# Kernel tuning notes

Measured on AMD Instinct MI355X. Metric: run time of the kernel, lower is better.

## Reference

```python
import jax, jax.numpy as jnp
import numpy as np

B, T, M, C, H = 2, 2048, 512, 512, 8
D = C // H
SCALE = 1.0 / np.sqrt(D).astype(np.float32)


def _linear_params(key, din, dout):
    kw, kb = jax.random.split(key)
    W = jax.random.normal(kw, (din, dout), jnp.float32) * 0.02
    b = jax.random.normal(kb, (dout,), jnp.float32) * 0.02
    return W, b


def setup_inputs() -> dict:
    key = jax.random.key(0)
    ks = jax.random.split(key, 8)
    x = jax.random.normal(ks[0], (B, T, C), jnp.float32)
    y = jax.random.normal(ks[1], (B, M, C), jnp.float32)
    # causal mask over the x (self / product-attn) axis, broadcasts to [B,H,T,T]
    attn_x_mask = jnp.tril(jnp.ones((T, T), jnp.int32))[None, None]
    Wqkv_x, bqkv_x = _linear_params(ks[2], C, 3 * C)
    Wqkv_y, bqkv_y = _linear_params(ks[3], C, 3 * C)
    Wgs, bgs = _linear_params(ks[4], C, C)
    Wgc, bgc = _linear_params(ks[5], C, C)
    Wp, bp = _linear_params(ks[6], C, C)
    return dict(x=x, y=y, attn_x_mask=attn_x_mask,
                Wqkv_x=Wqkv_x, bqkv_x=bqkv_x, Wqkv_y=Wqkv_y, bqkv_y=bqkv_y,
                Wgs=Wgs, bgs=bgs, Wgc=Wgc, bgc=bgc, Wp=Wp, bp=bp)


def _heads(t, L):
    # [B,L,C] -> [B,H,L,D]
    return t.reshape(B, L, H, D).transpose(0, 2, 1, 3)


def reference(x, y, attn_x_mask, Wqkv_x, bqkv_x, Wqkv_y, bqkv_y,
              Wgs, bgs, Wgc, bgc, Wp, bp):
    neg_inf = jnp.float32(-jnp.inf)
    qx, kx, vx = jnp.split(x @ Wqkv_x + bqkv_x, 3, axis=-1)
    qy, ky, vy = jnp.split(y @ Wqkv_y + bqkv_y, 3, axis=-1)
    q_x, k_x, v_x = _heads(qx, T), _heads(kx, T), _heads(vx, T)
    q_y, k_y, v_y = _heads(qy, M), _heads(ky, M), _heads(vy, M)

    # cross attention x -> y : [B,H,T,M]
    catt_x2y = jnp.einsum('bhtd,bhmd->bhtm', q_x, k_y) * SCALE
    cval_x2y = jnp.einsum('bhtm,bhmd->bhtd', jax.nn.softmax(catt_x2y, axis=-1), v_y)
    cval_x2y = cval_x2y.transpose(0, 2, 1, 3).reshape(B, T, C)

    # product attention: (x->y scores) @ (y->x scores) : [B,H,T,T]
    catt_y2x = jnp.einsum('bhmd,bhtd->bhmt', q_y, k_x) * SCALE
    prod = jnp.einsum('bhtm,bhms->bhts', catt_x2y, catt_y2x) * SCALE
    prod = jnp.where(attn_x_mask == 0, neg_inf, prod)
    cval_y2x = jnp.einsum('bhts,bhsd->bhtd', jax.nn.softmax(prod, axis=-1), v_x)
    cval_y2x = cval_y2x.transpose(0, 2, 1, 3).reshape(B, T, C)

    cval = cval_x2y + cval_y2x

    # self attention on x : [B,H,T,T]
    satt = jnp.einsum('bhtd,bhsd->bhts', q_x, k_x) * SCALE
    satt = jnp.where(attn_x_mask == 0, neg_inf, satt)
    sval = jnp.einsum('bhts,bhsd->bhtd', jax.nn.softmax(satt, axis=-1), v_x)
    sval = sval.transpose(0, 2, 1, 3).reshape(B, T, C)

    sgate = jax.nn.sigmoid(sval @ Wgs + bgs)
    cgate = jax.nn.sigmoid(cval @ Wgc + bgc)
    out = (sgate * cval + cgate * sval) @ Wp + bp
    return out
```

## Files before the change

kernel.cpp:

```cpp
#include <hip/hip_runtime.h>
#include <hip/hip_bf16.h>

typedef unsigned short ushort_t;
typedef __attribute__((ext_vector_type(8))) short s8v;
typedef __attribute__((ext_vector_type(4))) float f4;
typedef __attribute__((ext_vector_type(4))) unsigned short u16x4;

#define BB 2
#define TT 2048
#define MMM 512
#define CC 512
#define HH 8
#define DD 64
#define SCALE 0.125f
#define SCALE_L2E 0.18033688011112042f

__device__ __forceinline__ ushort_t f2bf(float v) {
    __hip_bfloat16 h = __float2bfloat16(v);
    return *reinterpret_cast<ushort_t*>(&h);
}
__device__ __forceinline__ float bf2f(ushort_t u) {
    __hip_bfloat16 h;
    *reinterpret_cast<ushort_t*>(&h) = u;
    return __bfloat162float(h);
// ... 135 lines not shown

    stage_rows128(Ab, 0, Al[0], w, lane);
    stage_rows128(Bb, 0, Bl[0], w, lane);
    __syncthreads();

    for (int kk = 0; kk < 8; ++kk) {
        const int cur = kk & 1;
        if (kk < 7) {
            stage_rows128(Ab, (kk + 1) * 64, Al[cur ^ 1], w, lane);
            stage_rows128(Bb, (kk + 1) * 64, Bl[cur ^ 1], w, lane);
        }
#pragma unroll
        for (int ks = 0; ks < 2; ++ks) {
            s8v af[4], bfr[4];
#pragma unroll
            for (int i = 0; i < 4; ++i) {
                int row = rowBase + 16 * i + l15;
                af[i] = *(const s8v*)&Al[cur][row * 64 + (((ks * 4 + quad) ^ (row & 7)) * 8)];
                int col = colBase + 16 * i + l15;
                bfr[i] = *(const s8v*)&Bl[cur][col * 64 + (((ks * 4 + quad) ^ (col & 7)) * 8)];
            }
#pragma unroll
            for (int i = 0; i < 4; ++i)
#pragma unroll
                for (int j = 0; j < 4; ++j)
                    acc[i][j] = __builtin_amdgcn_mfma_f32_16x16x32_bf16(af[i], bfr[j], acc[i][j], 0, 0, 0);
        }
        __syncthreads();
    }

#pragma unroll
    for (int i = 0; i < 4; ++i)
#pragma unroll
        for (int j = 0; j < 4; ++j)
#pragma unroll
            for (int r = 0; r < 4; ++r) {
                int row = r0 + rowBase + 16 * i + quad * 4 + r;
                int col = c0 + colBase + 16 * j + l15;
                float v = acc[i][j][r] + bias[col];
                if (col < qcols) v *= SCALE_L2E;
                O[(long)row * 1536 + col] = f2bf(v);
            }
}

__global__ __launch_bounds__(256) void proj_k(
    const ushort_t* __restrict__ A, const ushort_t* __restrict__ Bm,
    float* __restrict__ O, const float* __restrict__ bias)
{
    const int r0 = blockIdx.y * 64, c0 = blockIdx.x * 64;
    const int tid = threadIdx.x, w = tid >> 6, lane = tid & 63;
    const int quad = lane >> 4, l15 = lane & 15;
    const int rowBase = (w >> 1) * 32, colBase = (w & 1) * 32;

    __shared__ __align__(16) ushort_t Al[3][64 * 64];
    __shared__ __align__(16) ushort_t Bl[3][64 * 64];

    const ushort_t* Ab = A + (long)r0 * 512;
    const ushort_t* Bb = Bm + (long)c0 * 512;

    f4 acc[2][2] = {};

    stage_rows64(Ab, 0, Al[0], w, lane);
    stage_rows64(Bb, 0, Bl[0], w, lane);
    stage_rows64(Ab, 64, Al[1], w, lane);
    stage_rows64(Bb, 64, Bl[1], w, lane);

    int cur = 0;
    for (int kk = 0; kk < 8; ++kk) {
        if (kk + 1 < 8) asm volatile("s_waitcnt vmcnt(4)" ::: "memory");
        else            asm volatile("s_waitcnt vmcnt(0)" ::: "memory");
        asm volatile("s_barrier" ::: "memory");
        if (kk + 2 < 8) {
            int s = cur + 2; if (s >= 3) s -= 3;
            stage_rows64(Ab, (kk + 2) * 64, Al[s], w, lane);
            stage_rows64(Bb, (kk + 2) * 64, Bl[s], w, lane);
        }
#pragma unroll
        for (int ks = 0; ks < 2; ++ks) {
            s8v af[2], bfr[2];
#pragma unroll
            for (int i = 0; i < 2; ++i) {
                int row = rowBase + 16 * i + l15;
                af[i] = *(const s8v*)&Al[cur][row * 64 + (((ks * 4 + quad) ^ (row & 7)) * 8)];
                int col = colBase + 16 * i + l15;
                bfr[i] = *(const s8v*)&Bl[cur][col * 64 + (((ks * 4 + quad) ^ (col & 7)) * 8)];
            }
#pragma unroll
            for (int i = 0; i < 2; ++i)
#pragma unroll
                for (int j = 0; j < 2; ++j)
                    acc[i][j] = __builtin_amdgcn_mfma_f32_16x16x32_bf16(af[i], bfr[j], acc[i][j], 0, 0, 0);
        }
        if (++cur == 3) cur = 0;
    }

#pragma unroll
    for (int i = 0; i < 2; ++i)
#pragma unroll
        for (int j = 0; j < 2; ++j)
#pragma unroll
            for (int r = 0; r < 4; ++r) {
                int row = r0 + rowBase + 16 * i + quad * 4 + r;
                int col = c0 + colBase + 16 * j + l15;
                O[(long)row * 512 + col] = acc[i][j][r] + bias[col];
            }
}

__global__ __launch_bounds__(256) void gt_k(const ushort_t* __restrict__ qyT,
                                            const ushort_t* __restrict__ kyT,
                                            ushort_t* __restrict__ Gt)
{
    const int z = blockIdx.x;
    const int tid = threadIdx.x, w = tid >> 6, lane = tid & 63;
    const int quad = lane >> 4, l15 = lane & 15;
    const ushort_t* A  = qyT + (long)z * 64 * MMM;
    const ushort_t* Bm = kyT + (long)z * 64 * MMM;
    __shared__ float red[4][4096];
    f4 acc[4][4] = {};
    for (int kk = 0; kk < 4; ++kk) {
        const int ks = w * 4 + kk;
        s8v af[4], bfr[4];
#pragma unroll
        for (int i = 0; i < 4; ++i) {
            af[i]  = *(const s8v*)(A  + (long)(16 * i + l15) * MMM + ks * 32 + quad * 8);
            bfr[i] = *(const s8v*)(Bm + (long)(16 * i + l15) * MMM + ks * 32 + quad * 8);
        }
#pragma unroll
        for (int i = 0; i < 4; ++i)
#pragma unroll
            for (int j = 0; j < 4; ++j)
                acc[i][j] = __builtin_amdgcn_mfma_f32_16x16x32_bf16(af[i], bfr[j], acc[i][j], 0, 0, 0);
    }
#pragma unroll
    for (int i = 0; i < 4; ++i)
#pragma unroll
        for (int j = 0; j < 4; ++j)
            *(f4*)&red[w][(i * 4 + j) * 256 + lane * 4] = acc[i][j];
    __syncthreads();
    const float s2 = SCALE * SCALE;
#pragma unroll
    for (int j = 0; j < 4; ++j) {
        f4 s = *(const f4*)&red[0][(w * 4 + j) * 256 + lane * 4];
#pragma unroll
        for (int ww = 1; ww < 4; ++ww)
            s += *(const f4*)&red[ww][(w * 4 + j) * 256 + lane * 4];
#pragma unroll
        for (int r = 0; r < 4; ++r) {
            int d2 = 16 * w + quad * 4 + r, d1 = 16 * j + l15;
            Gt[(long)z * 4096 + d2 * 64 + d1] = f2bf(s2 * s[r]);
        }
    }
}

__device__ __forceinline__ void stage_k64(const ushort_t* src, long rstride, int s0,
                                          ushort_t* Kl, int w, int lane) {
#pragma unroll
    for (int n = 0; n < 2; ++n) {
        int f = w * 2048 + n * 1024 + lane * 16;
        int row = f >> 7;
        int krow = ((row & 15) << 2) | (row >> 4);
        int blk = ((f & 127) >> 4) ^ (row & 7);
        gload16(src + (long)(s0 + krow) * rstride + blk * 8, &Kl[(w * 2048 + n * 1024) >> 1]);
    }
}
__device__ __forceinline__ void stage_v64(const ushort_t* src, long rstride, int s0,
                                          ushort_t* Vl, int w, int lane) {
#pragma unroll
    for (int n = 0; n < 2; ++n) {
        int f = w * 2048 + n * 1024 + lane * 16;
        int row = f >> 7;
        int blk = ((f & 127) >> 4) ^ (row & 7);
        gload16(src + (long)row * rstride + s0 + blk * 8, &Vl[(w * 2048 + n * 1024) >> 1]);
    }
}
__device__ __forceinline__ void qk8(f4 Sc[4], const s8v qf[2], const ushort_t* Kl,
                                    int quad, int l15) {
    __builtin_amdgcn_s_setprio(1);
#pragma unroll
    for (int ks = 0; ks < 2; ++ks)
#pragma unroll
        for (int c = 0; c < 4; ++c) {
            int row = 16 * c + l15;
            s8v bb = *(const s8v*)&Kl[row * 64 + (((ks * 4 + quad) ^ (row & 7)) * 8)];
            Sc[c] = __builtin_amdgcn_mfma_f32_16x16x32_bf16(qf[ks], bb, Sc[c], 0, 0, 0);
        }
    __builtin_amdgcn_s_setprio(0);
}
__device__ __forceinline__ void qk8_dual(f4 Ss[4], f4 Sp[4], const s8v qa[2], const s8v qb[2],
                                         const ushort_t* Kl, int quad, int l15) {
    __builtin_amdgcn_s_setprio(1);
#pragma unroll
    for (int ks = 0; ks < 2; ++ks)
#pragma unroll
        for (int c = 0; c < 4; ++c) {
            int row = 16 * c + l15;
            s8v bb = *(const s8v*)&Kl[row * 64 + (((ks * 4 + quad) ^ (row & 7)) * 8)];
            Ss[c] = __builtin_amdgcn_mfma_f32_16x16x32_bf16(qa[ks], bb, Ss[c], 0, 0, 0);
            Sp[c] = __builtin_amdgcn_mfma_f32_16x16x32_bf16(qb[ks], bb, Sp[c], 0, 0, 0);
        }
    __builtin_amdgcn_s_setprio(0);
}
__device__ __forceinline__ void smax0(const f4 Sc[4], float l_i[4], ushort_t* PlW,
                                      int diag, int trow0, int s0, int quad, int l15) {
#pragma unroll
    for (int r = 0; r < 4; ++r) {
        const int trow = trow0 + quad * 4 + r;
        u16x4 o;
#pragma unroll
        for (int c = 0; c < 4; ++c) {
            float v = Sc[c][r];
            if (diag && (s0 + 4 * l15 + c) > trow) v = -3e38f;
            float p = exp2_raw(v);
            l_i[r] += p;
            o[c] = f2bf(p);
        }
        *(u16x4*)&PlW[(quad * 4 + r) * 72 + 4 * l15] = o;
    }
}
__device__ __forceinline__ void pv8(f4 Oc[4], const ushort_t* PlW, const ushort_t* Vl,
                                    int quad, int l15) {
    __builtin_amdgcn_s_setprio(1);
#pragma unroll
    for (int ks = 0; ks < 2; ++ks) {
        s8v a = *(const s8v*)&PlW[l15 * 72 + ks * 32 + quad * 8];
#pragma unroll
        for (int c = 0; c < 4; ++c) {
            int row = 16 * c + l15;
            s8v bb = *(const s8v*)&Vl[row * 64 + (((ks * 4 + quad) ^ (row & 7)) * 8)];
            Oc[c] = __builtin_amdgcn_mfma_f32_16x16x32_bf16(a, bb, Oc[c], 0, 0, 0);
        }
    }
    __builtin_amdgcn_s_setprio(0);
}
__device__ __forceinline__ void pv8_dual(f4 Os[4], f4 Op[4], const ushort_t* Ps,
                                         const ushort_t* Pp, const ushort_t* Vl,
                                         int quad, int l15) {
    __builtin_amdgcn_s_setprio(1);
#pragma unroll
    for (int ks = 0; ks < 2; ++ks) {
        s8v as = *(const s8v*)&Ps[l15 * 72 + ks * 32 + quad * 8];
        s8v ap = *(const s8v*)&Pp[l15 * 72 + ks * 32 + quad * 8];
#pragma unroll
        for (int c = 0; c < 4; ++c) {
            int row = 16 * c + l15;
            s8v bb = *(const s8v*)&Vl[row * 64 + (((ks * 4 + quad) ^ (row & 7)) * 8)];
            Os[c] = __builtin_amdgcn_mfma_f32_16x16x32_bf16(as, bb, Os[c], 0, 0, 0);
            Op[c] = __builtin_amdgcn_mfma_f32_16x16x32_bf16(ap, bb, Op[c], 0, 0, 0);
        }
    }
    __builtin_amdgcn_s_setprio(0);
}

__global__ __launch_bounds__(256, 2) void flash_fused(
    const ushort_t* __restrict__ qkvx, const ushort_t* __restrict__ qkvy,
    const ushort_t* __restrict__ Gt, const ushort_t* __restrict__ vxT,
    const ushort_t* __restrict__ vyT,
    ushort_t* __restrict__ cval, ushort_t* __restrict__ sval)
{
    const int z = blockIdx.y, b = z >> 3, h = z & 7;
    const ushort_t* qx = qkvx + (long)b * (TT * 1536) + h * 64;
    const ushort_t* kx = qx + 512;
    const ushort_t* ky = qkvy + (long)b * (MMM * 1536) + 512 + h * 64;
    const ushort_t* Gz = Gt + (long)z * 4096;
    const ushort_t* vx = vxT + (long)z * (64 * TT);
    const ushort_t* vy = vyT + (long)z * (64 * MMM);

    const int xw = (z & 8) ? (int)blockIdx.x : (int)(gridDim.x - 1 - blockIdx.x);
    const int t0 = xw * 64;
    const int tid = threadIdx.x, w = tid >> 6, lane = tid & 63;
    const int quad = lane >> 4, l15 = lane & 15;

    __shared__ __align__(16) ushort_t Kl[3][64 * 64];
    __shared__ __align__(16) ushort_t Vl[3][64 * 64];
    __shared__ __align__(16) ushort_t Pl[2][4 * 16 * 72];
    ushort_t* PlWs = &Pl[0][w * 1152];
    ushort_t* PlWp = &Pl[1][w * 1152];

    stage_k64(ky, 1536, 0, Kl[0], w, lane);
    stage_v64(vy, MMM, 0, Vl[0], w, lane);
    stage_k64(ky, 1536, 64, Kl[1], w, lane);
    stage_v64(vy, MMM, 64, Vl[1], w, lane);

    const int qrow = t0 + 16 * w + l15;
    s8v qfx[2], qft[2];
    qfx[0] = *(const s8v*)(qx + (long)qrow * 1536 + quad * 8);
    qfx[1] = *(const s8v*)(qx + (long)qrow * 1536 + 32 + quad * 8);
    {
        f4 qa[4] = {};
#pragma unroll
        for (int ks = 0; ks < 2; ++ks)
#pragma unroll
            for (int j = 0; j < 4; ++j) {
                s8v bb = *(const s8v*)(Gz + (4 * l15 + j) * 64 + ks * 32 + quad * 8);
                qa[j] = __builtin_amdgcn_mfma_f32_16x16x32_bf16(qfx[ks], bb, qa[j], 0, 0, 0);
            }
#pragma unroll
        for (int r = 0; r < 4; ++r) {
            u16x4 o;
#pragma unroll
            for (int j = 0; j < 4; ++j) o[j] = f2bf(qa[j][r]);
            *(u16x4*)&PlWs[(quad * 4 + r) * 72 + 4 * l15] = o;
        }
        qft[0] = *(const s8v*)&PlWs[l15 * 72 + quad * 8];
        qft[1] = *(const s8v*)&PlWs[l15 * 72 + 32 + quad * 8];
    }

    f4 Occ[4] = {}, Ocs[4] = {}, Ocp[4] = {};
    float lc[4] = {}, ls[4] = {}, lp[4] = {};

    const int nT1 = MMM / 64;
    const int nTiles = nT1 + t0 / 64 + 1;

    int cur = 0;
    for (int ti = 0; ti < nTiles; ++ti) {
        if (ti + 1 < nTiles) asm volatile("s_waitcnt vmcnt(4)" ::: "memory");
        else                 asm volatile("s_waitcnt vmcnt(0)" ::: "memory");
        asm volatile("s_barrier" ::: "memory");
        if (ti + 2 < nTiles) {
            int s = cur + 2; if (s >= 3) s -= 3;
            const int tn = ti + 2;
            if (tn < nT1) {
                stage_k64(ky, 1536, tn * 64, Kl[s], w, lane);
                stage_v64(vy, MMM, tn * 64, Vl[s], w, lane);
            } else {
                const int s0n = (tn - nT1) * 64;
                stage_k64(kx, 1536, s0n, Kl[s], w, lane);
                stage_v64(vx, TT, s0n, Vl[s], w, lane);
            }
        }
        if (ti < nT1) {
            f4 Sc[4] = {};
            qk8(Sc, qfx, Kl[cur], quad, l15);
            smax0(Sc, lc, PlWs, 0, 0, 0, quad, l15);
            pv8(Occ, PlWs, Vl[cur], quad, l15);
        } else {
            const int s0 = (ti - nT1) * 64;
            const int diag = (s0 == t0);
            f4 Ss[4] = {}, Sp[4] = {};
            qk8_dual(Ss, Sp, qfx, qft, Kl[cur], quad, l15);
            smax0(Ss, ls, PlWs, diag, t0 + 16 * w, s0, quad, l15);
            smax0(Sp, lp, PlWp, diag, t0 + 16 * w, s0, quad, l15);
            pv8_dual(Ocs, Ocp, PlWs, PlWp, Vl[cur], quad, l15);
        }
        if (++cur == 3) cur = 0;
    }

#pragma unroll
    for (int r = 0; r < 4; ++r)
#pragma unroll
        for (int mb = 1; mb < 16; mb <<= 1) {
            lc[r] += __shfl_xor(lc[r], mb, 64);
            ls[r] += __shfl_xor(ls[r], mb, 64);
            lp[r] += __shfl_xor(lp[r], mb, 64);
        }

    const long ob = (long)b * (TT * CC) + h * 64;
#pragma unroll
    for (int r = 0; r < 4; ++r) {
        int row = t0 + 16 * w + quad * 4 + r;
        float ic = 1.f / lc[r], ip = 1.f / lp[r], isv = 1.f / ls[r];
#pragma unroll
        for (int c = 0; c < 4; ++c) {
            long idx = ob + (long)row * CC + 16 * c + l15;
            cval[idx] = f2bf(Occ[c][r] * ic + Ocp[c][r] * ip);
            sval[idx] = f2bf(Ocs[c][r] * isv);
        }
    }
}

__global__ __launch_bounds__(256) void gate_gemm(
    const ushort_t* __restrict__ sval, const ushort_t* __restrict__ cvalb,
    const ushort_t* __restrict__ WgsT, const ushort_t* __restrict__ WgcT,
    const float* __restrict__ bgs, const float* __restrict__ bgc,
    ushort_t* __restrict__ tmpb)
{
    const int r0 = blockIdx.y * 64, c0 = blockIdx.x * 64;
    const int tid = threadIdx.x, w = tid >> 6, lane = tid & 63;
    const int quad = lane >> 4, l15 = lane & 15;
    const int rowBase = (w >> 1) * 32, colBase = (w & 1) * 32;

    __shared__ __align__(16) ushort_t Al[3][64 * 64];
    __shared__ __align__(16) ushort_t Bl[3][64 * 64];

    const ushort_t* Ap[2] = { sval + (long)r0 * 512, cvalb + (long)r0 * 512 };
    const ushort_t* Bp[2] = { WgsT + (long)c0 * 512, WgcT + (long)c0 * 512 };

    f4 acc1[2][2] = {}, acc2[2][2] = {};

    stage_rows64(Ap[0], 0, Al[0], w, lane);
    stage_rows64(Bp[0], 0, Bl[0], w, lane);
    stage_rows64(Ap[0], 64, Al[1], w, lane);
    stage_rows64(Bp[0], 64, Bl[1], w, lane);

    int cur = 0;
    for (int st = 0; st < 16; ++st) {
        if (st + 1 < 16) asm volatile("s_waitcnt vmcnt(4)" ::: "memory");
        else             asm volatile("s_waitcnt vmcnt(0)" ::: "memory");
        asm volatile("s_barrier" ::: "memory");
        if (st + 2 < 16) {
            int s = cur + 2; if (s >= 3) s -= 3;
            const int nx = st + 2, p = nx >> 3;
            stage_rows64(Ap[p], (nx & 7) * 64, Al[s], w, lane);
            stage_rows64(Bp[p], (nx & 7) * 64, Bl[s], w, lane);
        }
#pragma unroll
        for (int ks = 0; ks < 2; ++ks) {
            s8v af[2], bfr[2];
#pragma unroll
            for (int i = 0; i < 2; ++i) {
                int row = rowBase + 16 * i + l15;
                af[i] = *(const s8v*)&Al[cur][row * 64 + (((ks * 4 + quad) ^ (row & 7)) * 8)];
                int col = colBase + 16 * i + l15;
                bfr[i] = *(const s8v*)&Bl[cur][col * 64 + (((ks * 4 + quad) ^ (col & 7)) * 8)];
            }
            if (st < 8) {
#pragma unroll
                for (int i = 0; i < 2; ++i)
#pragma unroll
                    for (int j = 0; j < 2; ++j)
                        acc1[i][j] = __builtin_amdgcn_mfma_f32_16x16x32_bf16(af[i], bfr[j], acc1[i][j], 0, 0, 0);
            } else {
#pragma unroll
                for (int i = 0; i < 2; ++i)
#pragma unroll
                    for (int j = 0; j < 2; ++j)
                        acc2[i][j] = __builtin_amdgcn_mfma_f32_16x16x32_bf16(af[i], bfr[j], acc2[i][j], 0, 0, 0);
            }
        }
        if (++cur == 3) cur = 0;
    }

#pragma unroll
    for (int i = 0; i < 2; ++i)
#pragma unroll
        for (int j = 0; j < 2; ++j)
#pragma unroll
            for (int r = 0; r < 4; ++r) {
                int row = r0 + rowBase + 16 * i + quad * 4 + r;
                int col = c0 + colBase + 16 * j + l15;
                long idx = (long)row * 512 + col;
                float g1 = 1.f / (1.f + __expf(-(acc1[i][j][r] + bgs[col])));
                float g2 = 1.f / (1.f + __expf(-(acc2[i][j][r] + bgc[col])));
                tmpb[idx] = f2bf(g1 * bf2f(cvalb[idx]) + g2 * bf2f(sval[idx]));
            }
}

extern "C" void kernel_launch(void* const* d_in, const int* in_sizes, int n_in,
                              void* d_out, int out_size, void* d_ws, size_t ws_size,
                              hipStream_t stream) {
    const float* x      = (const float*)d_in[0];
    const float* y      = (const float*)d_in[1];
    const float* Wqkv_x = (const float*)d_in[3];
    const float* bqkv_x = (const float*)d_in[4];
    const float* Wqkv_y = (const float*)d_in[5];
    const float* bqkv_y = (const float*)d_in[6];
    const float* Wgs    = (const float*)d_in[7];
    const float* bgs    = (const float*)d_in[8];
    const float* Wgc    = (const float*)d_in[9];
    const float* bgc    = (const float*)d_in[10];
    const float* Wp     = (const float*)d_in[11];
    const float* bp     = (const float*)d_in[12];
    float* out = (float*)d_out;

    ushort_t* u = (ushort_t*)d_ws;
    long o = 0;
    ushort_t* xb    = u + o; o += (long)BB * TT * CC;
    ushort_t* yb    = u + o; o += (long)BB * MMM * CC;
    ushort_t* WqxT  = u + o; o += 1536L * 512;
    ushort_t* WqyT  = u + o; o += 1536L * 512;
    ushort_t* WgsT  = u + o; o += 512L * 512;
    ushort_t* WgcT  = u + o; o += 512L * 512;
    ushort_t* WpT   = u + o; o += 512L * 512;
    ushort_t* qkvx  = u + o; o += (long)BB * TT * 1536;
    ushort_t* qkvy  = u + o; o += (long)BB * MMM * 1536;
    ushort_t* vxT   = u + o; o += (long)BB * HH * DD * TT;
    ushort_t* vyT   = u + o; o += (long)BB * HH * DD * MMM;
    ushort_t* kyT   = u + o; o += (long)BB * HH * DD * MMM;
    ushort_t* qyT   = u + o; o += (long)BB * HH * DD * MMM;
    ushort_t* Gt    = u + o; o += 16L * 64 * 64;
    ushort_t* cvalb = u + o; o += (long)BB * TT * CC;
    ushort_t* sval  = u + o; o += (long)BB * TT * CC;
    ushort_t* tmpb  = u + o; o += (long)BB * TT * CC;

    dim3 blk(256);

    prep_k<<<dim3(4864), blk, 0, stream>>>(x, y, Wqkv_x, Wqkv_y, Wgs, Wgc, Wp,
                                           xb, yb, WqxT, WqyT, WgsT, WgcT, WpT);

    qkv_k<<<dim3(12, 40), blk, 0, stream>>>(xb, yb, WqxT, WqyT, bqkv_x, bqkv_y, qkvx, qkvy);

    vT_fused<<<dim3(56, 16), blk, 0, stream>>>(qkvx, qkvy, vxT, vyT, kyT, qyT);

    gt_k<<<dim3(16), blk, 0, stream>>>(qyT, kyT, Gt);

    flash_fused<<<dim3(32, 16), blk, 0, stream>>>(qkvx, qkvy, Gt, vxT, vyT, cvalb, sval);

    gate_gemm<<<dim3(8, 64), blk, 0, stream>>>(sval, cvalb, WgsT, WgcT, bgs, bgc, tmpb);

    proj_k<<<dim3(8, 64), blk, 0, stream>>>(tmpb, WpT, out, bp);
}
```

Baseline: 206.6 us.

## Balance causal flash work by pairing query tiles and splitting long tiles

Each block now handles a short query tile (qA) plus part of its mirrored long tile (qB = 31 - p), so every block processes the same number of KV tiles. The long tile's work is split across two blocks, which write unnormalized partial outputs and row sums to fp32 scratch. A new combine kernel sums the two partials, normalizes, and writes cval and sval. This targets tail imbalance from the causal triangle, at the cost of an extra launch, fp32 partial traffic, and a second Q-fragment and Gt setup per block.

```diff
diff --git a/kernel.cpp b/kernel.cpp
--- a/kernel.cpp
+++ b/kernel.cpp
@@ -409,14 +409,111 @@
     }
     __builtin_amdgcn_s_setprio(0);
 }
+__device__ __forceinline__ void reduce16(float (&a)[4], float (&b)[4], float (&c)[4]) {
+#pragma unroll
+    for (int r = 0; r < 4; ++r)
+#pragma unroll
+        for (int mb = 1; mb < 16; mb <<= 1) {
+            a[r] += __shfl_xor(a[r], mb, 64);
+            b[r] += __shfl_xor(b[r], mb, 64);
+            c[r] += __shfl_xor(c[r], mb, 64);
+        }
+}
+
+__device__ __forceinline__ void run_chunk(
+    const ushort_t* ky, const ushort_t* vy, const ushort_t* kx, const ushort_t* vx,
+    const ushort_t* qx, const ushort_t* Gz,
+    ushort_t (*Kl)[64 * 64], ushort_t (*Vl)[64 * 64],
+    ushort_t* PlWs, ushort_t* PlWp,
+    int qt, int c0, int nc, int u0, int nu,
+    int w, int lane, int quad, int l15,
+    f4 (&Occ)[4], f4 (&Ocs)[4], f4 (&Ocp)[4],
+    float (&lc)[4], float (&ls)[4], float (&lp)[4])
+{
+    const int n = nc + nu;
+    const int t0q = qt * 64;
+    auto stage = [&](int ti, int slot) {
+        if (ti < nc) {
+            const int c = c0 + ti;
+            stage_k64(ky, 1536, c * 64, Kl[slot], w, lane);
+            stage_v64(vy, MMM, c * 64, Vl[slot], w, lane);
+        } else {
+            const int uu = u0 + ti - nc;
+            stage_k64(kx, 1536, uu * 64, Kl[slot], w, lane);
+            stage_v64(vx, TT, uu * 64, Vl[slot], w, lane);
+        }
+    };
+    stage(0, 0);
+    stage(1, 1);
+
+    const int qrow = t0q + 16 * w + l15;
+    s8v qfx[2], qft[2];
+    qfx[0] = *(const s8v*)(qx + (long)qrow * 1536 + quad * 8);
+    qfx[1] = *(const s8v*)(qx + (long)qrow * 1536 + 32 + quad * 8);
+    if (nu > 0) {
+        f4 qa[4] = {};
+#pragma unroll
+        for (int ks = 0; ks < 2; ++ks)
+#pragma unroll
+            for (int j = 0; j < 4; ++j) {
+                s8v bb = *(const s8v*)(Gz + (4 * l15 + j) * 64 + ks * 32 + quad * 8);
+                qa[j] = __builtin_amdgcn_mfma_f32_16x16x32_bf16(qfx[ks], bb, qa[j], 0, 0, 0);
+            }
+#pragma unroll
+        for (int r = 0; r < 4; ++r) {
+            u16x4 o;
+#pragma unroll
+            for (int j = 0; j < 4; ++j) o[j] = f2bf(qa[j][r]);
+            *(u16x4*)&PlWs[(quad * 4 + r) * 72 + 4 * l15] = o;
+        }
+        qft[0] = *(const s8v*)&PlWs[l15 * 72 + quad * 8];
+        qft[1] = *(const s8v*)&PlWs[l15 * 72 + 32 + quad * 8];
+    } else {
+        qft[0] = qfx[0]; qft[1] = qfx[1];
+    }
+    asm volatile("s_waitcnt vmcnt(0)" ::: "memory");
+    asm volatile("s_barrier" ::: "memory");
+
+    int cur = 0;
+    for (int ti = 0; ti < n; ++ti) {
+        if (ti > 0) {
+            if (ti + 1 < n) asm volatile("s_waitcnt vmcnt(4)" ::: "memory");
+            else            asm volatile("s_waitcnt vmcnt(0)" ::: "memory");
+            asm volatile("s_barrier" ::: "memory");
+        }
+        if (ti + 2 < n) {
+            int sl = cur + 2; if (sl >= 3) sl -= 3;
+            stage(ti + 2, sl);
+        }
+        if (ti < nc) {
+            f4 Sc[4] = {};
+            qk8(Sc, qfx, Kl[cur], quad, l15);
+            smax0(Sc, lc, PlWs, 0, 0, 0, quad, l15);
+            pv8(Occ, PlWs, Vl[cur], quad, l15);
+        } else {
+            const int uu = u0 + ti - nc;
+            const int diag = (uu == qt);
+            f4 Ss[4] = {}, Sp[4] = {};
+            qk8_dual(Ss, Sp, qfx, qft, Kl[cur], quad, l15);
+            smax0(Ss, ls, PlWs, diag, t0q + 16 * w, uu * 64, quad, l15);
+            smax0(Sp, lp, PlWp, diag, t0q + 16 * w, uu * 64, quad, l15);
+            pv8_dual(Ocs, Ocp, PlWs, PlWp, Vl[cur], quad, l15);
+        }
+        if (++cur == 3) cur = 0;
+    }
+    asm volatile("s_barrier" ::: "memory");
+}
 
 __global__ __launch_bounds__(256, 2) void flash_fused(
     const ushort_t* __restrict__ qkvx, const ushort_t* __restrict__ qkvy,
     const ushort_t* __restrict__ Gt, const ushort_t* __restrict__ vxT,
     const ushort_t* __restrict__ vyT,
-    ushort_t* __restrict__ cval, ushort_t* __restrict__ sval)
+    ushort_t* __restrict__ cval, ushort_t* __restrict__ sval,
+    float* __restrict__ partO, float* __restrict__ partL)
 {
     const int z = blockIdx.y, b = z >> 3, h = z & 7;
+    const int sblk = blockIdx.x, p = sblk >> 1, half = sblk & 1;
+    const int qA = p, qB = 31 - p;
     const ushort_t* qx = qkvx + (long)b * (TT * 1536) + h * 64;
     const ushort_t* kx = qx + 512;
     const ushort_t* ky = qkvy + (long)b * (MMM * 1536) + 512 + h * 64;
@@ -424,8 +521,6 @@
     const ushort_t* vx = vxT + (long)z * (64 * TT);
     const ushort_t* vy = vyT + (long)z * (64 * MMM);
 
-    const int xw = (z & 8) ? (int)blockIdx.x : (int)(gridDim.x - 1 - blockIdx.x);
-    const int t0 = xw * 64;
     const int tid = threadIdx.x, w = tid >> 6, lane = tid & 63;
     const int quad = lane >> 4, l15 = lane & 15;
 
@@ -435,95 +530,111 @@
     ushort_t* PlWs = &Pl[0][w * 1152];
     ushort_t* PlWp = &Pl[1][w * 1152];
 
-    stage_k64(ky, 1536, 0, Kl[0], w, lane);
-    stage_v64(vy, MMM, 0, Vl[0], w, lane);
-    stage_k64(ky, 1536, 64, Kl[1], w, lane);
-    stage_v64(vy, MMM, 64, Vl[1], w, lane);
-
-    const int qrow = t0 + 16 * w + l15;
-    s8v qfx[2], qft[2];
-    qfx[0] = *(const s8v*)(qx + (long)qrow * 1536 + quad * 8);
-    qfx[1] = *(const s8v*)(qx + (long)qrow * 1536 + 32 + quad * 8);
-    {
-        f4 qa[4] = {};
-#pragma unroll
-        for (int ks = 0; ks < 2; ++ks)
-#pragma unroll
-            for (int j = 0; j < 4; ++j) {
-                s8v bb = *(const s8v*)(Gz + (4 * l15 + j) * 64 + ks * 32 + quad * 8);
-                qa[j] = __builtin_amdgcn_mfma_f32_16x16x32_bf16(qfx[ks], bb, qa[j], 0, 0, 0);
-            }
+    int cA2, uA2;
+    if (p >= 12) { cA2 = 32 - 2 * p; uA2 = 0; }
+    else         { cA2 = 8;          uA2 = 12 - p; }
+
+    const long obase = (long)b * (TT * CC) + h * 64;
+    const long inst = (long)z * 16 + (qB - 16);
+    float* po = partO + (inst * 2 + half) * 3 * 4096;
+    float* pl = partL + (inst * 2 + half) * 3 * 64;
+
+    if (half == 0) {
+        {
+            f4 Occ[4] = {}, Ocs[4] = {}, Ocp[4] = {};
+            float lc[4] = {}, ls[4] = {}, lp[4] = {};
+            run_chunk(ky, vy, kx, vx, qx, Gz, Kl, Vl, PlWs, PlWp,
+                      qA, 0, 8, 0, qA + 1, w, lane, quad, l15,
+                      Occ, Ocs, Ocp, lc, ls, lp);
+            reduce16(lc, ls, lp);
+#pragma unroll
+            for (int r = 0; r < 4; ++r) {
+                int row = qA * 64 + 16 * w + quad * 4 + r;
+                float ic = 1.f / lc[r], ip = 1.f / lp[r], isv = 1.f / ls[r];
+#pragma unroll
+                for (int c = 0; c < 4; ++c) {
+                    long idx = obase + (long)row * CC + 16 * c + l15;
+                    cval[idx] = f2bf(Occ[c][r] * ic + Ocp[c][r] * ip);
+                    sval[idx] = f2bf(Ocs[c][r] * isv);
+                }
+            }
+        }
+        {
+            f4 Occ[4] = {}, Ocs[4] = {}, Ocp[4] = {};
+            float lc[4] = {}, ls[4] = {}, lp[4] = {};
+            run_chunk(ky, vy, kx, vx, qx, Gz, Kl, Vl, PlWs, PlWp,
+                      qB, 0, cA2, 0, uA2, w, lane, quad, l15,
+                      Occ, Ocs, Ocp, lc, ls, lp);
+            reduce16(lc, ls, lp);
+#pragma unroll
+            for (int r = 0; r < 4; ++r) {
+                const int row = 16 * w + quad * 4 + r;
+#pragma unroll
+                for (int c = 0; c < 4; ++c) {
+                    const int col = 16 * c + l15;
+                    po[row * 64 + col]        = Occ[c][r];
+                    po[4096 + row * 64 + col] = Ocs[c][r];
+                    po[8192 + row * 64 + col] = Ocp[c][r];
+                }
+                if (l15 == 0) { pl[row] = lc[r]; pl[64 + row] = ls[r]; pl[128 + row] = lp[r]; }
+            }
+        }
+    } else {
+        f4 Occ[4] = {}, Ocs[4] = {}, Ocp[4] = {};
+        float lc[4] = {}, ls[4] = {}, lp[4] = {};
+        run_chunk(ky, vy, kx, vx, qx, Gz, Kl, Vl, PlWs, PlWp,
+                  qB, cA2, 8 - cA2, uA2, (qB + 1) - uA2, w, lane, quad, l15,
+                  Occ, Ocs, Ocp, lc, ls, lp);
+        reduce16(lc, ls, lp);
 #pragma unroll
         for (int r = 0; r < 4; ++r) {
-            u16x4 o;
-#pragma unroll
-            for (int j = 0; j < 4; ++j) o[j] = f2bf(qa[j][r]);
-            *(u16x4*)&PlWs[(quad * 4 + r) * 72 + 4 * l15] = o;
-        }
-        qft[0] = *(const s8v*)&PlWs[l15 * 72 + quad * 8];
-        qft[1] = *(const s8v*)&PlWs[l15 * 72 + 32 + quad * 8];
-    }
-
-    f4 Occ[4] = {}, Ocs[4] = {}, Ocp[4] = {};
-    float lc[4] = {}, ls[4] = {}, lp[4] = {};
-
-    const int nT1 = MMM / 64;
-    const int nTiles = nT1 + t0 / 64 + 1;
-
-    int cur = 0;
-    for (int ti = 0; ti < nTiles; ++ti) {
-        if (ti + 1 < nTiles) asm volatile("s_waitcnt vmcnt(4)" ::: "memory");
-        else                 asm volatile("s_waitcnt vmcnt(0)" ::: "memory");
-        asm volatile("s_barrier" ::: "memory");
-        if (ti + 2 < nTiles) {
-            int s = cur + 2; if (s >= 3) s -= 3;
-            const int tn = ti + 2;
-            if (tn < nT1) {
-                stage_k64(ky, 1536, tn * 64, Kl[s], w, lane);
-                stage_v64(vy, MMM, tn * 64, Vl[s], w, lane);
-            } else {
-                const int s0n = (tn - nT1) * 64;
-                stage_k64(kx, 1536, s0n, Kl[s], w, lane);
-                stage_v64(vx, TT, s0n, Vl[s], w, lane);
-            }
-        }
-        if (ti < nT1) {
-            f4 Sc[4] = {};
-            qk8(Sc, qfx, Kl[cur], quad, l15);
-            smax0(Sc, lc, PlWs, 0, 0, 0, quad, l15);
-            pv8(Occ, PlWs, Vl[cur], quad, l15);
-        } else {
-            const int s0 = (ti - nT1) * 64;
-            const int diag = (s0 == t0);
-            f4 Ss[4] = {}, Sp[4] = {};
-            qk8_dual(Ss, Sp, qfx, qft, Kl[cur], quad, l15);
-            smax0(Ss, ls, PlWs, diag, t0 + 16 * w, s0, quad, l15);
-            smax0(Sp, lp, PlWp, diag, t0 + 16 * w, s0, quad, l15);
-            pv8_dual(Ocs, Ocp, PlWs, PlWp, Vl[cur], quad, l15);
-        }
-        if (++cur == 3) cur = 0;
-    }
-
-#pragma unroll
-    for (int r = 0; r < 4; ++r)
-#pragma unroll
-        for (int mb = 1; mb < 16; mb <<= 1) {
-            lc[r] += __shfl_xor(lc[r], mb, 64);
-            ls[r] += __shfl_xor(ls[r], mb, 64);
-            lp[r] += __shfl_xor(lp[r], mb, 64);
-        }
-
-    const long ob = (long)b * (TT * CC) + h * 64;
-#pragma unroll
-    for (int r = 0; r < 4; ++r) {
-        int row = t0 + 16 * w + quad * 4 + r;
-        float ic = 1.f / lc[r], ip = 1.f / lp[r], isv = 1.f / ls[r];
-#pragma unroll
-        for (int c = 0; c < 4; ++c) {
-            long idx = ob + (long)row * CC + 16 * c + l15;
-            cval[idx] = f2bf(Occ[c][r] * ic + Ocp[c][r] * ip);
-            sval[idx] = f2bf(Ocs[c][r] * isv);
-        }
+            const int row = 16 * w + quad * 4 + r;
+#pragma unroll
+            for (int c = 0; c < 4; ++c) {
+                const int col = 16 * c + l15;
+                po[row * 64 + col]        = Occ[c][r];
+                po[4096 + row * 64 + col] = Ocs[c][r];
+                po[8192 + row * 64 + col] = Ocp[c][r];
+            }
+            if (l15 == 0) { pl[row] = lc[r]; pl[64 + row] = ls[r]; pl[128 + row] = lp[r]; }
+        }
+    }
+}
+
+__global__ __launch_bounds__(256) void combine_k(
+    const float* __restrict__ partO, const float* __restrict__ partL,
+    ushort_t* __restrict__ cval, ushort_t* __restrict__ sval)
+{
+    const int inst = blockIdx.x;
+    const int z = inst >> 4, qb = 16 + (inst & 15);
+    const int b = z >> 3, h = z & 7;
+    const int tid = threadIdx.x;
+    const int row = tid >> 2, cq = (tid & 3) * 16;
+    const float* p0 = partO + ((long)inst * 2 + 0) * 3 * 4096;
+    const float* p1 = partO + ((long)inst * 2 + 1) * 3 * 4096;
+    const float* l0 = partL + ((long)inst * 2 + 0) * 3 * 64;
+    const float* l1 = partL + ((long)inst * 2 + 1) * 3 * 64;
+    const float ic  = 1.f / (l0[row] + l1[row]);
+    const float isv = 1.f / (l0[64 + row] + l1[64 + row]);
+    const float ip  = 1.f / (l0[128 + row] + l1[128 + row]);
+    const long ob = (long)b * (TT * CC) + h * 64 + (long)(qb * 64 + row) * CC + cq;
+    u16x4 vc[4], vs[4];
+#pragma unroll
+    for (int k = 0; k < 4; ++k) {
+        const int e = row * 64 + cq + k * 4;
+        f4 oc = *(const f4*)&p0[e]        + *(const f4*)&p1[e];
+        f4 os = *(const f4*)&p0[4096 + e] + *(const f4*)&p1[4096 + e];
+        f4 op = *(const f4*)&p0[8192 + e] + *(const f4*)&p1[8192 + e];
+#pragma unroll
+        for (int j = 0; j < 4; ++j) {
+            vc[k][j] = f2bf(oc[j] * ic + op[j] * ip);
+            vs[k][j] = f2bf(os[j] * isv);
+        }
+    }
+#pragma unroll
+    for (int k = 0; k < 4; ++k) {
+        *(u16x4*)&cval[ob + k * 4] = vc[k];
+        *(u16x4*)&sval[ob + k * 4] = vs[k];
     }
 }
 
@@ -640,6 +751,8 @@
     ushort_t* cvalb = u + o; o += (long)BB * TT * CC;
     ushort_t* sval  = u + o; o += (long)BB * TT * CC;
     ushort_t* tmpb  = u + o; o += (long)BB * TT * CC;
+    float* partO = (float*)(u + o); o += 256L * 2 * 3 * 4096 * 2;
+    float* partL = (float*)(u + o); o += 256L * 2 * 3 * 64 * 2;
 
     dim3 blk(256);
 
@@ -652,7 +765,10 @@
 
     gt_k<<<dim3(16), blk, 0, stream>>>(qyT, kyT, Gt);
 
-    flash_fused<<<dim3(32, 16), blk, 0, stream>>>(qkvx, qkvy, Gt, vxT, vyT, cvalb, sval);
+    flash_fused<<<dim3(32, 16), blk, 0, stream>>>(qkvx, qkvy, Gt, vxT, vyT,
+                                                  cvalb, sval, partO, partL);
+
+    combine_k<<<dim3(256), blk, 0, stream>>>(partO, partL, cvalb, sval);
 
     gate_gemm<<<dim3(8, 64), blk, 0, stream>>>(sval, cvalb, WgsT, WgcT, bgs, bgc, tmpb);
 
```

Measured after the change: 218.3 us. 1.06x slower.

## Pair causal query tiles per 512-thread block to balance flash attention work

Applied to the files above, without the earlier changes.

The flash kernel now runs 512-thread blocks in which two 4-wave groups handle query tiles p and 31-p, so every block does the same amount of causal work. The groups share the K/V tiles staged in LDS. Past the shorter tile's diagonal, group 0 switches to the self-attention half of the longer tile while group 1 handles the product half, and the partial accumulators are combined through LDS at the end. This targets the load imbalance of the triangular causal loop and cuts redundant K/V loads for the shared y-tiles, at the cost of a more complex schedule and fewer blocks in flight.

```diff
diff --git a/kernel.cpp b/kernel.cpp
--- a/kernel.cpp
+++ b/kernel.cpp
@@ -311,26 +311,20 @@
     }
 }
 
-__device__ __forceinline__ void stage_k64(const ushort_t* src, long rstride, int s0,
-                                          ushort_t* Kl, int w, int lane) {
-#pragma unroll
-    for (int n = 0; n < 2; ++n) {
-        int f = w * 2048 + n * 1024 + lane * 16;
-        int row = f >> 7;
-        int krow = ((row & 15) << 2) | (row >> 4);
-        int blk = ((f & 127) >> 4) ^ (row & 7);
-        gload16(src + (long)(s0 + krow) * rstride + blk * 8, &Kl[(w * 2048 + n * 1024) >> 1]);
-    }
-}
-__device__ __forceinline__ void stage_v64(const ushort_t* src, long rstride, int s0,
-                                          ushort_t* Vl, int w, int lane) {
-#pragma unroll
-    for (int n = 0; n < 2; ++n) {
-        int f = w * 2048 + n * 1024 + lane * 16;
-        int row = f >> 7;
-        int blk = ((f & 127) >> 4) ^ (row & 7);
-        gload16(src + (long)row * rstride + s0 + blk * 8, &Vl[(w * 2048 + n * 1024) >> 1]);
-    }
+__device__ __forceinline__ void stage_k8(const ushort_t* src, long rstride, int s0,
+                                         ushort_t* Kl, int w2, int lane) {
+    int f = w2 * 1024 + lane * 16;
+    int row = f >> 7;
+    int krow = ((row & 15) << 2) | (row >> 4);
+    int blk = ((f & 127) >> 4) ^ (row & 7);
+    gload16(src + (long)(s0 + krow) * rstride + blk * 8, &Kl[(w2 * 1024) >> 1]);
+}
+__device__ __forceinline__ void stage_v8(const ushort_t* src, long rstride, int s0,
+                                         ushort_t* Vl, int w2, int lane) {
+    int f = w2 * 1024 + lane * 16;
+    int row = f >> 7;
+    int blk = ((f & 127) >> 4) ^ (row & 7);
+    gload16(src + (long)row * rstride + s0 + blk * 8, &Vl[(w2 * 1024) >> 1]);
 }
 __device__ __forceinline__ void qk8(f4 Sc[4], const s8v qf[2], const ushort_t* Kl,
                                     int quad, int l15) {
@@ -409,14 +403,25 @@
     }
     __builtin_amdgcn_s_setprio(0);
 }
-
-__global__ __launch_bounds__(256, 2) void flash_fused(
+__device__ __forceinline__ void reduce16(float (&a)[4], float (&b)[4], float (&c)[4]) {
+#pragma unroll
+    for (int r = 0; r < 4; ++r)
+#pragma unroll
+        for (int mb = 1; mb < 16; mb <<= 1) {
+            a[r] += __shfl_xor(a[r], mb, 64);
+            b[r] += __shfl_xor(b[r], mb, 64);
+            c[r] += __shfl_xor(c[r], mb, 64);
+        }
+}
+
+__global__ __launch_bounds__(512, 2) void flash_fused(
     const ushort_t* __restrict__ qkvx, const ushort_t* __restrict__ qkvy,
     const ushort_t* __restrict__ Gt, const ushort_t* __restrict__ vxT,
     const ushort_t* __restrict__ vyT,
     ushort_t* __restrict__ cval, ushort_t* __restrict__ sval)
 {
     const int z = blockIdx.y, b = z >> 3, h = z & 7;
+    const int p = blockIdx.x;
     const ushort_t* qx = qkvx + (long)b * (TT * 1536) + h * 64;
     const ushort_t* kx = qx + 512;
     const ushort_t* ky = qkvy + (long)b * (MMM * 1536) + 512 + h * 64;
@@ -424,27 +429,28 @@
     const ushort_t* vx = vxT + (long)z * (64 * TT);
     const ushort_t* vy = vyT + (long)z * (64 * MMM);
 
-    const int xw = (z & 8) ? (int)blockIdx.x : (int)(gridDim.x - 1 - blockIdx.x);
-    const int t0 = xw * 64;
-    const int tid = threadIdx.x, w = tid >> 6, lane = tid & 63;
+    const int tid = threadIdx.x, w2 = tid >> 6, lane = tid & 63;
+    const int g = w2 >> 2, w = w2 & 3;
     const int quad = lane >> 4, l15 = lane & 15;
+    const int qB = 31 - p;
+    const int qg = g ? qB : p;
 
     __shared__ __align__(16) ushort_t Kl[3][64 * 64];
     __shared__ __align__(16) ushort_t Vl[3][64 * 64];
-    __shared__ __align__(16) ushort_t Pl[2][4 * 16 * 72];
-    ushort_t* PlWs = &Pl[0][w * 1152];
-    ushort_t* PlWp = &Pl[1][w * 1152];
-
-    stage_k64(ky, 1536, 0, Kl[0], w, lane);
-    stage_v64(vy, MMM, 0, Vl[0], w, lane);
-    stage_k64(ky, 1536, 64, Kl[1], w, lane);
-    stage_v64(vy, MMM, 64, Vl[1], w, lane);
-
-    const int qrow = t0 + 16 * w + l15;
+    __shared__ __align__(16) ushort_t Pl[2][8 * 16 * 72];
+    ushort_t* PlWs = &Pl[0][w2 * 1152];
+    ushort_t* PlWp = &Pl[1][w2 * 1152];
+
+    stage_k8(ky, 1536, 0, Kl[0], w2, lane);
+    stage_v8(vy, MMM, 0, Vl[0], w2, lane);
+    stage_k8(ky, 1536, 64, Kl[1], w2, lane);
+    stage_v8(vy, MMM, 64, Vl[1], w2, lane);
+
     s8v qfx[2], qft[2];
-    qfx[0] = *(const s8v*)(qx + (long)qrow * 1536 + quad * 8);
-    qfx[1] = *(const s8v*)(qx + (long)qrow * 1536 + 32 + quad * 8);
     {
+        const int qrow = qg * 64 + 16 * w + l15;
+        qfx[0] = *(const s8v*)(qx + (long)qrow * 1536 + quad * 8);
+        qfx[1] = *(const s8v*)(qx + (long)qrow * 1536 + 32 + quad * 8);
         f4 qa[4] = {};
 #pragma unroll
         for (int ks = 0; ks < 2; ++ks)
@@ -463,66 +469,112 @@
         qft[0] = *(const s8v*)&PlWs[l15 * 72 + quad * 8];
         qft[1] = *(const s8v*)&PlWs[l15 * 72 + 32 + quad * 8];
     }
+    asm volatile("s_waitcnt vmcnt(0)" ::: "memory");
+    asm volatile("s_barrier" ::: "memory");
 
     f4 Occ[4] = {}, Ocs[4] = {}, Ocp[4] = {};
     float lc[4] = {}, ls[4] = {}, lp[4] = {};
 
-    const int nT1 = MMM / 64;
-    const int nTiles = nT1 + t0 / 64 + 1;
-
+    const long obase = (long)b * (TT * CC) + h * 64;
+    const int n = 40 - p;
     int cur = 0;
-    for (int ti = 0; ti < nTiles; ++ti) {
-        if (ti + 1 < nTiles) asm volatile("s_waitcnt vmcnt(4)" ::: "memory");
-        else                 asm volatile("s_waitcnt vmcnt(0)" ::: "memory");
-        asm volatile("s_barrier" ::: "memory");
-        if (ti + 2 < nTiles) {
+    for (int ti = 0; ti < n; ++ti) {
+        if (ti > 0) {
+            if (ti + 1 < n) asm volatile("s_waitcnt vmcnt(2)" ::: "memory");
+            else            asm volatile("s_waitcnt vmcnt(0)" ::: "memory");
+            asm volatile("s_barrier" ::: "memory");
+        }
+        if (ti + 2 < n) {
             int s = cur + 2; if (s >= 3) s -= 3;
             const int tn = ti + 2;
-            if (tn < nT1) {
-                stage_k64(ky, 1536, tn * 64, Kl[s], w, lane);
-                stage_v64(vy, MMM, tn * 64, Vl[s], w, lane);
+            if (tn < 8) {
+                stage_k8(ky, 1536, tn * 64, Kl[s], w2, lane);
+                stage_v8(vy, MMM, tn * 64, Vl[s], w2, lane);
             } else {
-                const int s0n = (tn - nT1) * 64;
-                stage_k64(kx, 1536, s0n, Kl[s], w, lane);
-                stage_v64(vx, TT, s0n, Vl[s], w, lane);
-            }
-        }
-        if (ti < nT1) {
+                const int u = tn - 8;
+                stage_k8(kx, 1536, u * 64, Kl[s], w2, lane);
+                stage_v8(vx, TT, u * 64, Vl[s], w2, lane);
+            }
+        }
+        if (ti < 8) {
             f4 Sc[4] = {};
             qk8(Sc, qfx, Kl[cur], quad, l15);
             smax0(Sc, lc, PlWs, 0, 0, 0, quad, l15);
             pv8(Occ, PlWs, Vl[cur], quad, l15);
         } else {
-            const int s0 = (ti - nT1) * 64;
-            const int diag = (s0 == t0);
-            f4 Ss[4] = {}, Sp[4] = {};
-            qk8_dual(Ss, Sp, qfx, qft, Kl[cur], quad, l15);
-            smax0(Ss, ls, PlWs, diag, t0 + 16 * w, s0, quad, l15);
-            smax0(Sp, lp, PlWp, diag, t0 + 16 * w, s0, quad, l15);
-            pv8_dual(Ocs, Ocp, PlWs, PlWp, Vl[cur], quad, l15);
+            const int u = ti - 8;
+            if (u <= p) {
+                const int diag = (u == qg);
+                f4 Ss[4] = {}, Sp[4] = {};
+                qk8_dual(Ss, Sp, qfx, qft, Kl[cur], quad, l15);
+                smax0(Ss, ls, PlWs, diag, qg * 64 + 16 * w, u * 64, quad, l15);
+                smax0(Sp, lp, PlWp, diag, qg * 64 + 16 * w, u * 64, quad, l15);
+                pv8_dual(Ocs, Ocp, PlWs, PlWp, Vl[cur], quad, l15);
+            } else {
+                const int diag = (u == qB);
+                if (g == 0) {
+                    f4 Ss[4] = {};
+                    qk8(Ss, qfx, Kl[cur], quad, l15);
+                    smax0(Ss, ls, PlWs, diag, qB * 64 + 16 * w, u * 64, quad, l15);
+                    pv8(Ocs, PlWs, Vl[cur], quad, l15);
+                } else {
+                    f4 Sp[4] = {};
+                    qk8(Sp, qft, Kl[cur], quad, l15);
+                    smax0(Sp, lp, PlWp, diag, qB * 64 + 16 * w, u * 64, quad, l15);
+                    pv8(Ocp, PlWp, Vl[cur], quad, l15);
+                }
+            }
+            if (u == p && g == 0) {
+                reduce16(lc, ls, lp);
+#pragma unroll
+                for (int r = 0; r < 4; ++r) {
+                    int row = p * 64 + 16 * w + quad * 4 + r;
+                    float ic = 1.f / lc[r], ip = 1.f / lp[r], isv = 1.f / ls[r];
+#pragma unroll
+                    for (int c = 0; c < 4; ++c) {
+                        long idx = obase + (long)row * CC + 16 * c + l15;
+                        cval[idx] = f2bf(Occ[c][r] * ic + Ocp[c][r] * ip);
+                        sval[idx] = f2bf(Ocs[c][r] * isv);
+                    }
+                }
+#pragma unroll
+                for (int c = 0; c < 4; ++c) Ocs[c] = f4{};
+#pragma unroll
+                for (int r = 0; r < 4; ++r) ls[r] = 0.f;
+                const int qrow2 = qB * 64 + 16 * w + l15;
+                qfx[0] = *(const s8v*)(qx + (long)qrow2 * 1536 + quad * 8);
+                qfx[1] = *(const s8v*)(qx + (long)qrow2 * 1536 + 32 + quad * 8);
+            }
         }
         if (++cur == 3) cur = 0;
     }
 
-#pragma unroll
-    for (int r = 0; r < 4; ++r)
-#pragma unroll
-        for (int mb = 1; mb < 16; mb <<= 1) {
-            lc[r] += __shfl_xor(lc[r], mb, 64);
-            ls[r] += __shfl_xor(ls[r], mb, 64);
-            lp[r] += __shfl_xor(lp[r], mb, 64);
-        }
-
-    const long ob = (long)b * (TT * CC) + h * 64;
-#pragma unroll
-    for (int r = 0; r < 4; ++r) {
-        int row = t0 + 16 * w + quad * 4 + r;
-        float ic = 1.f / lc[r], ip = 1.f / lp[r], isv = 1.f / ls[r];
-#pragma unroll
-        for (int c = 0; c < 4; ++c) {
-            long idx = ob + (long)row * CC + 16 * c + l15;
-            cval[idx] = f2bf(Occ[c][r] * ic + Ocp[c][r] * ip);
-            sval[idx] = f2bf(Ocs[c][r] * isv);
+    __syncthreads();
+    float* comb = (float*)&Kl[0][0];
+    const int cbase = (w * 64 + lane) * 20;
+    if (g == 0) {
+#pragma unroll
+        for (int c = 0; c < 4; ++c) *(f4*)&comb[cbase + 4 * c] = Ocs[c];
+#pragma unroll
+        for (int r = 0; r < 4; ++r) comb[cbase + 16 + r] = ls[r];
+    }
+    __syncthreads();
+    if (g == 1) {
+#pragma unroll
+        for (int c = 0; c < 4; ++c) Ocs[c] += *(const f4*)&comb[cbase + 4 * c];
+#pragma unroll
+        for (int r = 0; r < 4; ++r) ls[r] += comb[cbase + 16 + r];
+        reduce16(lc, ls, lp);
+#pragma unroll
+        for (int r = 0; r < 4; ++r) {
+            int row = qB * 64 + 16 * w + quad * 4 + r;
+            float ic = 1.f / lc[r], ip = 1.f / lp[r], isv = 1.f / ls[r];
+#pragma unroll
+            for (int c = 0; c < 4; ++c) {
+                long idx = obase + (long)row * CC + 16 * c + l15;
+                cval[idx] = f2bf(Occ[c][r] * ic + Ocp[c][r] * ip);
+                sval[idx] = f2bf(Ocs[c][r] * isv);
+            }
         }
     }
 }
@@ -652,7 +704,8 @@
 
     gt_k<<<dim3(16), blk, 0, stream>>>(qyT, kyT, Gt);
 
-    flash_fused<<<dim3(32, 16), blk, 0, stream>>>(qkvx, qkvy, Gt, vxT, vyT, cvalb, sval);
+    flash_fused<<<dim3(16, 16), dim3(512), 0, stream>>>(qkvx, qkvy, Gt, vxT, vyT,
+                                                        cvalb, sval);
 
     gate_gemm<<<dim3(8, 64), blk, 0, stream>>>(sval, cvalb, WgsT, WgcT, bgs, bgc, tmpb);
 
```

New measurement: 215.8 us. 4.4% more time.

## Switch K/V staging to double buffer and preload V fragments into registers

Applied to the files above, without the earlier changes.

Reduces the shared K/V ring from three stages to two and replaces the manual vmcnt wait plus raw barrier with __syncthreads, prefetching only one tile ahead. V fragments are read from LDS into registers right after QK so their latency overlaps the softmax. The smaller LDS footprint may allow more resident blocks, but the shorter prefetch distance and the full syncthreads wait on every iteration can expose global-load latency. Holding the V fragments also raises register pressure.

```diff
diff --git a/kernel.cpp b/kernel.cpp
--- a/kernel.cpp
+++ b/kernel.cpp
@@ -359,6 +359,15 @@
         }
     __builtin_amdgcn_s_setprio(0);
 }
+__device__ __forceinline__ void vload8(s8v vf[8], const ushort_t* Vl, int quad, int l15) {
+#pragma unroll
+    for (int ks = 0; ks < 2; ++ks)
+#pragma unroll
+        for (int c = 0; c < 4; ++c) {
+            int row = 16 * c + l15;
+            vf[ks * 4 + c] = *(const s8v*)&Vl[row * 64 + (((ks * 4 + quad) ^ (row & 7)) * 8)];
+        }
+}
 __device__ __forceinline__ void smax0(const f4 Sc[4], float l_i[4], ushort_t* PlW,
                                       int diag, int trow0, int s0, int quad, int l15) {
 #pragma unroll
@@ -376,24 +385,21 @@
         *(u16x4*)&PlW[(quad * 4 + r) * 72 + 4 * l15] = o;
     }
 }
-__device__ __forceinline__ void pv8(f4 Oc[4], const ushort_t* PlW, const ushort_t* Vl,
-                                    int quad, int l15) {
+__device__ __forceinline__ void pv8r(f4 Oc[4], const ushort_t* PlW, const s8v vf[8],
+                                     int quad, int l15) {
     __builtin_amdgcn_s_setprio(1);
 #pragma unroll
     for (int ks = 0; ks < 2; ++ks) {
         s8v a = *(const s8v*)&PlW[l15 * 72 + ks * 32 + quad * 8];
 #pragma unroll
-        for (int c = 0; c < 4; ++c) {
-            int row = 16 * c + l15;
-            s8v bb = *(const s8v*)&Vl[row * 64 + (((ks * 4 + quad) ^ (row & 7)) * 8)];
-            Oc[c] = __builtin_amdgcn_mfma_f32_16x16x32_bf16(a, bb, Oc[c], 0, 0, 0);
-        }
+        for (int c = 0; c < 4; ++c)
+            Oc[c] = __builtin_amdgcn_mfma_f32_16x16x32_bf16(a, vf[ks * 4 + c], Oc[c], 0, 0, 0);
     }
     __builtin_amdgcn_s_setprio(0);
 }
-__device__ __forceinline__ void pv8_dual(f4 Os[4], f4 Op[4], const ushort_t* Ps,
-                                         const ushort_t* Pp, const ushort_t* Vl,
-                                         int quad, int l15) {
+__device__ __forceinline__ void pv8r_dual(f4 Os[4], f4 Op[4], const ushort_t* Ps,
+                                          const ushort_t* Pp, const s8v vf[8],
+                                          int quad, int l15) {
     __builtin_amdgcn_s_setprio(1);
 #pragma unroll
     for (int ks = 0; ks < 2; ++ks) {
@@ -401,10 +407,8 @@
         s8v ap = *(const s8v*)&Pp[l15 * 72 + ks * 32 + quad * 8];
 #pragma unroll
         for (int c = 0; c < 4; ++c) {
-            int row = 16 * c + l15;
-            s8v bb = *(const s8v*)&Vl[row * 64 + (((ks * 4 + quad) ^ (row & 7)) * 8)];
-            Os[c] = __builtin_amdgcn_mfma_f32_16x16x32_bf16(as, bb, Os[c], 0, 0, 0);
-            Op[c] = __builtin_amdgcn_mfma_f32_16x16x32_bf16(ap, bb, Op[c], 0, 0, 0);
+            Os[c] = __builtin_amdgcn_mfma_f32_16x16x32_bf16(as, vf[ks * 4 + c], Os[c], 0, 0, 0);
+            Op[c] = __builtin_amdgcn_mfma_f32_16x16x32_bf16(ap, vf[ks * 4 + c], Op[c], 0, 0, 0);
         }
     }
     __builtin_amdgcn_s_setprio(0);
@@ -429,16 +433,14 @@
     const int tid = threadIdx.x, w = tid >> 6, lane = tid & 63;
     const int quad = lane >> 4, l15 = lane & 15;
 
-    __shared__ __align__(16) ushort_t Kl[3][64 * 64];
-    __shared__ __align__(16) ushort_t Vl[3][64 * 64];
+    __shared__ __align__(16) ushort_t Kl[2][64 * 64];
+    __shared__ __align__(16) ushort_t Vl[2][64 * 64];
     __shared__ __align__(16) ushort_t Pl[2][4 * 16 * 72];
     ushort_t* PlWs = &Pl[0][w * 1152];
     ushort_t* PlWp = &Pl[1][w * 1152];
 
     stage_k64(ky, 1536, 0, Kl[0], w, lane);
     stage_v64(vy, MMM, 0, Vl[0], w, lane);
-    stage_k64(ky, 1536, 64, Kl[1], w, lane);
-    stage_v64(vy, MMM, 64, Vl[1], w, lane);
 
     const int qrow = t0 + 16 * w + l15;
     s8v qfx[2], qft[2];
@@ -470,38 +472,38 @@
     const int nT1 = MMM / 64;
     const int nTiles = nT1 + t0 / 64 + 1;
 
-    int cur = 0;
     for (int ti = 0; ti < nTiles; ++ti) {
-        if (ti + 1 < nTiles) asm volatile("s_waitcnt vmcnt(4)" ::: "memory");
-        else                 asm volatile("s_waitcnt vmcnt(0)" ::: "memory");
-        asm volatile("s_barrier" ::: "memory");
-        if (ti + 2 < nTiles) {
-            int s = cur + 2; if (s >= 3) s -= 3;
-            const int tn = ti + 2;
+        const int bi = ti & 1;
+        __syncthreads();
+        if (ti + 1 < nTiles) {
+            const int tn = ti + 1, bn = tn & 1;
             if (tn < nT1) {
-                stage_k64(ky, 1536, tn * 64, Kl[s], w, lane);
-                stage_v64(vy, MMM, tn * 64, Vl[s], w, lane);
+                stage_k64(ky, 1536, tn * 64, Kl[bn], w, lane);
+                stage_v64(vy, MMM, tn * 64, Vl[bn], w, lane);
             } else {
                 const int s0n = (tn - nT1) * 64;
-                stage_k64(kx, 1536, s0n, Kl[s], w, lane);
-                stage_v64(vx, TT, s0n, Vl[s], w, lane);
+                stage_k64(kx, 1536, s0n, Kl[bn], w, lane);
+                stage_v64(vx, TT, s0n, Vl[bn], w, lane);
             }
         }
         if (ti < nT1) {
             f4 Sc[4] = {};
-            qk8(Sc, qfx, Kl[cur], quad, l15);
+            qk8(Sc, qfx, Kl[bi], quad, l15);
+            s8v vf[8];
+            vload8(vf, Vl[bi], quad, l15);
             smax0(Sc, lc, PlWs, 0, 0, 0, quad, l15);
-            pv8(Occ, PlWs, Vl[cur], quad, l15);
+            pv8r(Occ, PlWs, vf, quad, l15);
         } else {
             const int s0 = (ti - nT1) * 64;
             const int diag = (s0 == t0);
             f4 Ss[4] = {}, Sp[4] = {};
-            qk8_dual(Ss, Sp, qfx, qft, Kl[cur], quad, l15);
+            qk8_dual(Ss, Sp, qfx, qft, Kl[bi], quad, l15);
+            s8v vf[8];
+            vload8(vf, Vl[bi], quad, l15);
             smax0(Ss, ls, PlWs, diag, t0 + 16 * w, s0, quad, l15);
             smax0(Sp, lp, PlWp, diag, t0 + 16 * w, s0, quad, l15);
-            pv8_dual(Ocs, Ocp, PlWs, PlWp, Vl[cur], quad, l15);
-        }
-        if (++cur == 3) cur = 0;
+            pv8r_dual(Ocs, Ocp, PlWs, PlWp, vf, quad, l15);
+        }
     }
 
 #pragma unroll
```

Measured after the change: 205.8 us. No clear change (-0.4%).
